# Kernel optimization log

Measured on AMD Instinct MI355X. Metric: run time of the kernel, lower is better.

The kernel has to match this reference:

```python
import jax, jax.numpy as jnp
import numpy as np

B, S, NH, HID, NL = 64, 512, 16, 512, 16
W_WIN, PAD, THR, BW = 5, 2, 5.0, 0.1
D_IN = 1 + 2 * NH


def setup_inputs():
    key = jax.random.key(0)
    ks = jax.random.split(key, 16)
    time = jax.random.uniform(ks[0], (B, S)) * 1000.0
    mag = 15.0 + jax.random.normal(ks[1], (B, S))
    err = 0.01 + 0.1 * jax.random.uniform(ks[2], (B, S))
    sc = 0.05
    p = {}
    p["light_curve"] = jnp.stack([time, mag, err], axis=1)  # (B,3,S)
    p["valid_mask"] = jnp.ones((B, S), dtype=bool)
    p["frequency"] = 0.5 + 4.5 * jax.random.uniform(ks[3], (B,))
    p["W_ih0"] = sc * jax.random.normal(ks[4], (3 * HID, D_IN))
    p["b_ih0"] = jnp.zeros((3 * HID,))
    p["W_hh0"] = sc * jax.random.normal(ks[5], (3 * HID, HID))
    p["b_hh0"] = jnp.zeros((3 * HID,))
    p["W_ih1"] = sc * jax.random.normal(ks[6], (3 * HID, HID))
    p["b_ih1"] = jnp.zeros((3 * HID,))
    p["W_hh1"] = sc * jax.random.normal(ks[7], (3 * HID, HID))
    p["b_hh1"] = jnp.zeros((3 * HID,))
    p["Wl1"] = sc * jax.random.normal(ks[8], (HID, HID))
    p["bl1"] = jnp.zeros((HID,))
    p["Wl2"] = sc * jax.random.normal(ks[9], (NL, HID))
    p["bl2"] = jnp.zeros((NL,))
    return p


def _flag_outliers(phase, mag):
    # Sorted-window weighted (Epanechnikov in circular phase-delta) mean/std outlier test.
    # Caller guarantees all points valid (setup uses an all-True mask), so index_select == identity.
    perm = jnp.argsort(phase)
    ps, ms = phase[perm], mag[perm]

    def windows(x):
        xp = jnp.concatenate([x[-PAD:], x, x[:PAD]])  # circular pad
        return jnp.stack([xp[i:i + S] for i in range(W_WIN)], axis=-1)  # (S, w)

    wp, wm = windows(ps), windows(ms)
    cols = jnp.array([i for i in range(W_WIN) if i != PAD])
    dphi = wp[:, cols] - wp[:, PAD:PAD + 1]
    dphi = jnp.remainder(dphi - 0.5, 1.0) - 0.5
    wgt = 0.75 * (1.0 - dphi ** 2)
    wmm = wm[:, cols]
    wsum = wgt.sum(-1)
    loc = (wmm * wgt).sum(-1) / wsum
    scale = jnp.sqrt((((wmm - loc[:, None]) ** 2) * wgt).sum(-1) / (wsum - 1.0))
    thr = loc + THR * scale
    sigma = jnp.zeros_like(mag).at[perm].set(thr)  # inverse-permute (index_copy_)
    return mag > sigma


def _gru_layer(x, W_ih, b_ih, W_hh, b_hh):
    # torch nn.GRU cell math; x: (B,S,D) -> (B,S,H)
    xW = jnp.einsum('bsd,gd->bsg', x, W_ih) + b_ih  # (B,S,3H)

    def step(h, xt):
        hW = h @ W_hh.T + b_hh
        xr, xz, xn = jnp.split(xt, 3, axis=-1)
        hr, hz, hn = jnp.split(hW, 3, axis=-1)
        r = jax.nn.sigmoid(xr + hr)
        z = jax.nn.sigmoid(xz + hz)
        n = jnp.tanh(xn + r * hn)
        h = (1.0 - z) * n + z * h
        return h, h

    h0 = jnp.zeros((x.shape[0], W_hh.shape[1]), x.dtype)
    _, hs = jax.lax.scan(step, h0, jnp.swapaxes(xW, 0, 1))
    return jnp.swapaxes(hs, 0, 1)


def reference(light_curve, valid_mask, frequency, W_ih0, b_ih0, W_hh0, b_hh0,
              W_ih1, b_ih1, W_hh1, b_hh1, Wl1, bl1, Wl2, bl2):
    time, mag, err = light_curve[:, 0], light_curve[:, 1], light_curve[:, 2]
    period = 2.0 / frequency[:, None]  # fold_with_double_period=True (default)
    phase = jnp.remainder(time, period) / period
    outlier = jax.vmap(_flag_outliers)(phase, mag)
    is_valid = valid_mask & ~outlier

    # periodic-kernel interpolation on 50-point grid; align phase to brightness max
    grid = jnp.linspace(0.0, 1.0, 50)
    delta = grid[None, :, None] - phase[:, None, :]  # (B,50,S)
    K = jnp.exp((jnp.cos(2.0 * jnp.pi * delta) - 1.0) / BW ** 2)
    Wk = is_valid[:, None, :].astype(K.dtype) * K
    Wk = Wk / Wk.sum(-1, keepdims=True)
    smooth = (Wk * mag[:, None, :]).sum(-1)  # (B,50)
    phase = phase - grid[jnp.argmax(smooth, axis=-1)][:, None]

    # sort by phase, invalid points last; scaler=None -> loc 0, scale 1
    big = jnp.finfo(jnp.float32).max
    idx = jnp.argsort(jnp.where(is_valid, phase, big), axis=-1)
    phase = jnp.take_along_axis(phase, idx, -1)
    mag = jnp.take_along_axis(mag, idx, -1)
    is_valid = jnp.take_along_axis(is_valid, idx, -1)

    # Fourier phase embedding [cos_1..cos_H, sin_1..sin_H] + mag -> (B,S,2H+1)
    k = jnp.arange(1, NH + 1, dtype=phase.dtype)
    ang = 2.0 * jnp.pi * phase[:, :, None] * k
    emb = jnp.concatenate([jnp.cos(ang), jnp.sin(ang), mag[:, :, None]], axis=-1)

    ht = _gru_layer(emb, W_ih0, b_ih0, W_hh0, b_hh0)
    ht = _gru_layer(ht, W_ih1, b_ih1, W_hh1, b_hh1)

    m = is_valid[:, :, None].astype(ht.dtype)  # context='average'
    ctx = (ht * m).sum(1) / m.sum(1)
    h1 = jax.nn.gelu(ctx @ Wl1.T + bl1, approximate=False)
    z = h1 @ Wl2.T + bl2
    return z
```

## Files before the change

### kernel.cpp

```cpp
#include <hip/hip_runtime.h>


typedef unsigned short u16;
typedef unsigned int u32;
typedef unsigned long long u64;

__device__ __forceinline__ float b2f(u16 u) { return __uint_as_float(((u32)u) << 16); }
__device__ __forceinline__ float blo(u32 u) { return __uint_as_float(u << 16); }
__device__ __forceinline__ float bhi(u32 u) { return __uint_as_float(u & 0xffff0000u); }
__device__ __forceinline__ u16 f2b(float f) {
    u32 x = __float_as_uint(f);
    u32 r = x + 0x7fffu + ((x >> 16) & 1u);
    return (u16)(r >> 16);
}

#define SS 512
#define TWO_PI 6.28318530717958647692f
#define BIGF 3.402823466e+38f
#define PANEL_ELEMS (1536 * 512)
#define FLAGS_BYTES 32768
#define FL(g, f) (((g) * 16 + (f)) * 16)
#define F_A 0
#define F_B 2
#define F_C 4
#define G_A 6
#define G_B 8
#define G_C 10
#define F_PRE 12
#define F_CTX 14

struct P {
    const void* lc;
    const void* freq;
    const void* W[12];
    void* out;
    void* ws;
    unsigned long long ws_size;
};

__device__ __forceinline__ bool inputs_are_bf16(const void* freq) {
    const u16* q = (const u16*)freq;
    bool ok = true;
    for (int i = 0; i < 64; ++i) {
        float v = b2f(q[i]);
        ok = ok && (v >= 0.4f) && (v <= 5.5f);
    }
    return ok;
}

template<bool BF>
__device__ __forceinline__ float ldw(const void* p, size_t i) {
    if constexpr (BF) return b2f(((const u16*)p)[i]);
    else              return ((const float*)p)[i];
}
template<bool BF>
__device__ __forceinline__ const void* rowp(const void* base, int row) {
    if constexpr (BF) return (const void*)((const u16*)base + (size_t)row * 512);
    else              return (const void*)((const float*)base + (size_t)row * 512);
}

__device__ __forceinline__ void sc_store_f(float* ptr, float v) {
    __hip_atomic_store(ptr, v, __ATOMIC_RELAXED, __HIP_MEMORY_SCOPE_AGENT);
}
__device__ __forceinline__ float sc_load_f(const float* ptr) {
    return __hip_atomic_load(ptr, __ATOMIC_RELAXED, __HIP_MEMORY_SCOPE_AGENT);
}
__device__ __forceinline__ void sc_store_i(int* ptr, int v) {
    __hip_atomic_store(ptr, v, __ATOMIC_RELAXED, __HIP_MEMORY_SCOPE_AGENT);
}
__device__ __forceinline__ int sc_load_i(const int* ptr) {
    return __hip_atomic_load(ptr, __ATOMIC_RELAXED, __HIP_MEMORY_SCOPE_AGENT);
}
__device__ __forceinline__ void waitge(const int* f, int v, int* dead) {
    if (*dead) return;
    int it = 0;
    while (sc_load_i(f) < v) {
        __builtin_amdgcn_s_sleep(1);
        if (++it > 2000000) { *dead = 1; break; }
    }
}

template<bool BF>
__device__ void build_panel_one(const void* W, int tid, char* panbase) {
    if constexpr (BF) {
        const uint4* Ws = (const uint4*)W;
        uint4* panel = (uint4*)panbase;
        for (int i = tid; i < 1536 * 64; i += 512) {
            int r = i >> 6, k8 = i & 63;
            panel[(size_t)k8 * 1536 + r] = Ws[i];
        }
    } else {
        const float4* Ws = (const float4*)W;
        float4* panel = (float4*)panbase;
        for (int i = tid; i < 1536 * 128; i += 512) {
            int r = i >> 7, k4 = i & 127;
            panel[(size_t)k4 * 1536 + r] = Ws[i];
        }
    }
}
template<bool BF>
__device__ void build_piece(const void* W, int half, int tid, char* panbase) {
    if constexpr (BF) {
        const uint4* Ws = (const uint4*)W;
        uint4* panel = (uint4*)panbase;
        for (int i = tid; i < 768 * 64; i += 512) {
            int r768 = i >> 6, k8 = i & 63;
            int g3 = r768 >> 8, r = r768 & 255;
            int srcrow = g3 * 512 + half * 256 + r;
            panel[(size_t)k8 * 768 + r768] = Ws[(size_t)srcrow * 64 + k8];
        }
    } else {
        const float4* Ws = (const float4*)W;
        float4* panel = (float4*)panbase;
        for (int i = tid; i < 768 * 128; i += 512) {
            int r768 = i >> 7, k4 = i & 127;
            int g3 = r768 >> 8, r = r768 & 255;
            int srcrow = g3 * 512 + half * 256 + r;
            panel[(size_t)k4 * 768 + r768] = Ws[(size_t)srcrow * 128 + k4];
        }
    }
}

template<bool BF>
__device__ __forceinline__ void tridot_panel(const void* panel, int j,
                                             const float* __restrict__ sh,
                                             float& ar, float& az, float& an) {
    if constexpr (BF) {
        const uint4* pr = (const uint4*)panel + j;
        const uint4* pz = pr + 512;
        const uint4* pn = pr + 1024;
        for (int k0 = 0; k0 < 512; k0 += 8) {
            size_t o = (size_t)(k0 >> 3) * 1536;
            float4 h0 = *(const float4*)&sh[k0];
            float4 h1 = *(const float4*)&sh[k0 + 4];
            uint4 a = pr[o], c = pz[o], d = pn[o];
            ar += blo(a.x) * h0.x + bhi(a.x) * h0.y + blo(a.y) * h0.z + bhi(a.y) * h0.w
                + blo(a.z) * h1.x + bhi(a.z) * h1.y + blo(a.w) * h1.z + bhi(a.w) * h1.w;
            az += blo(c.x) * h0.x + bhi(c.x) * h0.y + blo(c.y) * h0.z + bhi(c.y) * h0.w
                + blo(c.z) * h1.x + bhi(c.z) * h1.y + blo(c.w) * h1.z + bhi(c.w) * h1.w;
            an += blo(d.x) * h0.x + bhi(d.x) * h0.y + blo(d.y) * h0.z + bhi(d.y) * h0.w
                + blo(d.z) * h1.x + bhi(d.z) * h1.y + blo(d.w) * h1.z + bhi(d.w) * h1.w;
        }
    } else {
        const float4* pr = (const float4*)panel + j;
        const float4* pz = pr + 512;
        const float4* pn = pr + 1024;
        for (int k0 = 0; k0 < 512; k0 += 8) {
            size_t o = (size_t)(k0 >> 2) * 1536;
            float4 h0 = *(const float4*)&sh[k0];
            float4 h1 = *(const float4*)&sh[k0 + 4];
            float4 a0 = pr[o], a1 = pr[o + 1536];
            float4 c0 = pz[o], c1 = pz[o + 1536];
            float4 d0 = pn[o], d1 = pn[o + 1536];
            ar += a0.x * h0.x + a0.y * h0.y + a0.z * h0.z + a0.w * h0.w
                + a1.x * h1.x + a1.y * h1.y + a1.z * h1.z + a1.w * h1.w;
            az += c0.x * h0.x + c0.y * h0.y + c0.z * h0.z + c0.w * h0.w
                + c1.x * h1.x + c1.y * h1.y + c1.z * h1.z + c1.w * h1.w;
            an += d0.x * h0.x + d0.y * h0.y + d0.z * h0.z + d0.w * h0.w
                + d1.x * h1.x + d1.y * h1.y + d1.z * h1.z + d1.w * h1.w;
        }
    }
}

template<bool BF>
__device__ __forceinline__ void tridot_piece(const void* panel, int r,
                                             const float* __restrict__ sh,
                                             float& ar, float& az, float& an) {
    if constexpr (BF) {
        const uint4* pr = (const uint4*)panel + r;
        const uint4* pz = pr + 256;
        const uint4* pn = pr + 512;
        for (int k0 = 0; k0 < 512; k0 += 8) {
            size_t o = (size_t)(k0 >> 3) * 768;
            float4 h0 = *(const float4*)&sh[k0];
            float4 h1 = *(const float4*)&sh[k0 + 4];
            uint4 a = pr[o], c = pz[o], d = pn[o];
            ar += blo(a.x) * h0.x + bhi(a.x) * h0.y + blo(a.y) * h0.z + bhi(a.y) * h0.w
                + blo(a.z) * h1.x + bhi(a.z) * h1.y + blo(a.w) * h1.z + bhi(a.w) * h1.w;
            az += blo(c.x) * h0.x + bhi(c.x) * h0.y + blo(c.y) * h0.z + bhi(c.y) * h0.w
                + blo(c.z) * h1.x + bhi(c.z) * h1.y + blo(c.w) * h1.z + bhi(c.w) * h1.w;
            an += blo(d.x) * h0.x + bhi(d.x) * h0.y + blo(d.y) * h0.z + bhi(d.y) * h0.w
                + blo(d.z) * h1.x + bhi(d.z) * h1.y + blo(d.w) * h1.z + bhi(d.w) * h1.w;
        }
    } else {
        const float4* pr = (const float4*)panel + r;
        const float4* pz = pr + 256;
        const float4* pn = pr + 512;
        for (int k0 = 0; k0 < 512; k0 += 8) {
            size_t o = (size_t)(k0 >> 2) * 768;
            float4 h0 = *(const float4*)&sh[k0];
            float4 h1 = *(const float4*)&sh[k0 + 4];
            float4 a0 = pr[o], a1 = pr[o + 768];
            float4 c0 = pz[o], c1 = pz[o + 768];
            float4 d0 = pn[o], d1 = pn[o + 768];
            ar += a0.x * h0.x + a0.y * h0.y + a0.z * h0.z + a0.w * h0.w
                + a1.x * h1.x + a1.y * h1.y + a1.z * h1.z + a1.w * h1.w;
            az += c0.x * h0.x + c0.y * h0.y + c0.z * h0.z + c0.w * h0.w
                + c1.x * h1.x + c1.y * h1.y + c1.z * h1.z + c1.w * h1.w;
            an += d0.x * h0.x + d0.y * h0.y + d0.z * h0.z + d0.w * h0.w
                + d1.x * h1.x + d1.y * h1.y + d1.z * h1.z + d1.w * h1.w;
        }
    }
}

template<bool BF>
__device__ __forceinline__ float dot512(const void* vr, const float* __restrict__ sh) {
    float acc = 0.f;
    if constexpr (BF) {
        const u32* pr = (const u32*)vr;
        for (int k0 = 0; k0 < 512; k0 += 8) {
            float4 h0 = *(const float4*)&sh[k0];
            float4 h1 = *(const float4*)&sh[k0 + 4];
            uint4 a = *(const uint4*)(pr + (k0 >> 1));
            acc += blo(a.x) * h0.x + bhi(a.x) * h0.y + blo(a.y) * h0.z + bhi(a.y) * h0.w
                 + blo(a.z) * h1.x + bhi(a.z) * h1.y + blo(a.w) * h1.z + bhi(a.w) * h1.w;
        }
    } else {
        const float* pr = (const float*)vr;
        for (int k0 = 0; k0 < 512; k0 += 8) {
            float4 h0 = *(const float4*)&sh[k0];
            float4 h1 = *(const float4*)&sh[k0 + 4];
            float4 a0 = *(const float4*)(pr + k0), a1 = *(const float4*)(pr + k0 + 4);
            acc += a0.x * h0.x + a0.y * h0.y + a0.z * h0.z + a0.w * h0.w
                 + a1.x * h1.x + a1.y * h1.y + a1.z * h1.z + a1.w * h1.w;
        }
    }
    return acc;
}

struct PreShm {
    float ph[512], mg[512], skey[512], sig[512], vld[512];
    int   sidx[512];
    float ps2[512], ms2[512], vs2[512];
    float pn[50][8], pd[50][8], smoothv[50];
    float gshift, nv;
};

__device__ void bitonic512(float* skey, int* sidx, int tid) {
    for (int k = 2; k <= 512; k <<= 1) {
        for (int j = k >> 1; j > 0; j >>= 1) {
            int ixj = tid ^ j;
            if (ixj > tid) {
                float ka = skey[tid], kb = skey[ixj];
                int ia = sidx[tid], ib = sidx[ixj];
                bool up = ((tid & k) == 0);
                bool agtb = (ka > kb) || (ka == kb && ia > ib);
                if (agtb == up) {
                    skey[tid] = kb; skey[ixj] = ka;
                    sidx[tid] = ib; sidx[ixj] = ia;
                }
            }
            __syncthreads();
        }
    }
}

template<bool BF>
__device__ void preproc_core(const P& p, PreShm& s, int b, int tid) {
    float period = 2.0f / ldw<BF>(p.freq, b);
    float t = ldw<BF>(p.lc, (size_t)b * 3 * SS + tid);
    float m = ldw<BF>(p.lc, (size_t)b * 3 * SS + SS + tid);
    float ph0 = fmodf(t, period) / period;
    s.ph[tid] = ph0; s.mg[tid] = m;
    s.skey[tid] = ph0; s.sidx[tid] = tid;
    __syncthreads();
    bitonic512(s.skey, s.sidx, tid);
    {
        float pc = s.skey[tid];
        float wv[4], mv[4];
        float wsum = 0.f, wm = 0.f;
        const int offs[4] = {-2, -1, 1, 2};
#pragma unroll
        for (int c = 0; c < 4; ++c) {
            int jj = (tid + offs[c]) & 511;
            float d = s.skey[jj] - pc;
            float u = d - 0.5f; u = u - floorf(u);
            float dphi = u - 0.5f;
            float w = 0.75f * (1.0f - dphi * dphi);
            float mm = s.mg[s.sidx[jj]];
            wv[c] = w; mv[c] = mm;
            wsum += w; wm += w * mm;
        }
        float loc = wm / wsum;
        float s2 = 0.f;
#pragma unroll
        for (int c = 0; c < 4; ++c) { float dm = mv[c] - loc; s2 += dm * dm * wv[c]; }
        float scale = sqrtf(s2 / (wsum - 1.0f));
        s.sig[s.sidx[tid]] = loc + 5.0f * scale;
    }
    __syncthreads();
    s.vld[tid] = (s.mg[tid] > s.sig[tid]) ? 0.0f : 1.0f;
    __syncthreads();
    if (tid == 0) {
        float acc = 0.f;
        for (int i = 0; i < 512; ++i) acc += s.vld[i];
        s.nv = acc;
    }
    {
        int g = tid >> 3, pq = tid & 7;
        if (g < 50) {
            float gv = (float)g * (1.0f / 49.0f);
            float num = 0.f, den = 0.f;
            int s0 = pq * 64;
            for (int ss = s0; ss < s0 + 64; ++ss) {
                float d = gv - s.ph[ss];
                float c = cosf(TWO_PI * d);
                float K = expf((c - 1.0f) * 100.0f);
                float w = s.vld[ss] * K;
                den += w; num += w * s.mg[ss];
            }
            s.pn[g][pq] = num; s.pd[g][pq] = den;
        }
    }
    __syncthreads();
    if (tid < 50) {
        float num = 0.f, den = 0.f;
#pragma unroll
        for (int c = 0; c < 8; ++c) { num += s.pn[tid][c]; den += s.pd[tid][c]; }
        s.smoothv[tid] = num / den;
    }
    __syncthreads();
    if (tid == 0) {
        float best = s.smoothv[0]; int bi = 0;
        for (int g = 1; g < 50; ++g) if (s.smoothv[g] > best) { best = s.smoothv[g]; bi = g; }
        s.gshift = (float)bi * (1.0f / 49.0f);
    }
    __syncthreads();
    float p2 = s.ph[tid] - s.gshift;
    s.ph[tid] = p2;
    s.skey[tid] = (s.vld[tid] > 0.f) ? p2 : BIGF;
    s.sidx[tid] = tid;
    __syncthreads();
    bitonic512(s.skey, s.sidx, tid);
    {
        int o = s.sidx[tid];
        s.ps2[tid] = s.ph[o]; s.ms2[tid] = s.mg[o]; s.vs2[tid] = s.vld[o];
    }
    __syncthreads();
}

struct ShmA { PreShm pre; float psb[2][512], msb[2][512]; float h0L[1024]; float eL[2][34]; };
struct ShmB { float h0loc[1024]; };
struct ShmC { float h1L[1024]; float vs2L[2][512]; float nvL[2]; float ctxL[512], gL[512]; };
struct ShmOldA { PreShm pre; float h0[512], h1[512], eL[34]; };
struct ShmU {
    union { ShmA a; ShmB b; ShmC c; ShmOldA o; } u;
    int dead;
};

template<bool BF, bool PAN>
__device__ void run_all(const P& p, ShmU& S) {
    PreShm& pre = S.u.o.pre;
    float* h0 = S.u.o.h0;
    float* h1 = S.u.o.h1;
    float* eL = S.u.o.eL;
    int b = blockIdx.x, tid = threadIdx.x;
    char* panbase = (char*)p.ws + FLAGS_BYTES;
    const size_t PMAT = (size_t)PANEL_ELEMS * (BF ? 2 : 4);

    if constexpr (PAN) {
        build_panel_one<BF>(p.W[2], tid, panbase);
        build_panel_one<BF>(p.W[4], tid, panbase + PMAT);
        build_panel_one<BF>(p.W[6], tid, panbase + 2 * PMAT);
        __threadfence();
    }
    preproc_core<BF>(p, pre, b, tid);

    int j = tid;
    float wr0[33], wz0[33], wn0[33];
#pragma unroll
    for (int d = 0; d < 33; ++d) {
        wr0[d] = ldw<BF>(p.W[0], (size_t)j * 33 + d);
        wz0[d] = ldw<BF>(p.W[0], ((size_t)j + 512) * 33 + d);
        wn0[d] = ldw<BF>(p.W[0], ((size_t)j + 1024) * 33 + d);
    }
    float bi0r = ldw<BF>(p.W[1], j), bi0z = ldw<BF>(p.W[1], j + 512), bi0n = ldw<BF>(p.W[1], j + 1024);
    float bh0r = ldw<BF>(p.W[3], j), bh0z = ldw<BF>(p.W[3], j + 512), bh0n = ldw<BF>(p.W[3], j + 1024);
    float bi1r = ldw<BF>(p.W[5], j), bi1z = ldw<BF>(p.W[5], j + 512), bi1n = ldw<BF>(p.W[5], j + 1024);
    float bh1r = ldw<BF>(p.W[7], j), bh1z = ldw<BF>(p.W[7], j + 512), bh1n = ldw<BF>(p.W[7], j + 1024);

    const void* pan0  = (const void*)panbase;
    const void* pan1x = (const void*)(panbase + PMAT);
    const void* pan1h = (const void*)(panbase + 2 * PMAT);
    const void *w0r = rowp<BF>(p.W[2], j), *w0z = rowp<BF>(p.W[2], j + 512), *w0n = rowp<BF>(p.W[2], j + 1024);
    const void *x1r = rowp<BF>(p.W[4], j), *x1z = rowp<BF>(p.W[4], j + 512), *x1n = rowp<BF>(p.W[4], j + 1024);
    const void *w1r = rowp<BF>(p.W[6], j), *w1z = rowp<BF>(p.W[6], j + 512), *w1n = rowp<BF>(p.W[6], j + 1024);

    h0[j] = 0.f; h1[j] = 0.f;
    float cacc = 0.f;
    __syncthreads();

    for (int tt = 0; tt < 512; ++tt) {
        if (j < 16) {
            float ang = TWO_PI * pre.ps2[tt] * (float)(j + 1);
            float sv, cv; sincosf(ang, &sv, &cv);
            eL[j] = cv; eL[16 + j] = sv;
        }
        if (j == 32) eL[32] = pre.ms2[tt];
        __syncthreads();
        float xr = bi0r, xz = bi0z, xn = bi0n;
#pragma unroll
        for (int d = 0; d < 33; ++d) {
            float e = eL[d];
            xr += wr0[d] * e; xz += wz0[d] * e; xn += wn0[d] * e;
        }
        float ar = bh0r, az = bh0z, an = bh0n;
        if constexpr (PAN) tridot_panel<BF>(pan0, j, h0, ar, az, an);
        else {
            for (int k = 0; k < 512; ++k) {
                float h = h0[k];
                ar += ldw<BF>(w0r, k) * h; az += ldw<BF>(w0z, k) * h; an += ldw<BF>(w0n, k) * h;
            }
        }
        float h0prev = h0[j];
        float r0 = 1.0f / (1.0f + expf(-(xr + ar)));
        float z0 = 1.0f / (1.0f + expf(-(xz + az)));
        float n0 = tanhf(xn + r0 * an);
        float nh0 = (1.0f - z0) * n0 + z0 * h0prev;
        __syncthreads();
        h0[j] = nh0;
        __syncthreads();
        float yr = bi1r, yz = bi1z, yn = bi1n;
        float cr = bh1r, cz = bh1z, cn = bh1n;
        if constexpr (PAN) {
            tridot_panel<BF>(pan1x, j, h0, yr, yz, yn);
            tridot_panel<BF>(pan1h, j, h1, cr, cz, cn);
        } else {
            for (int k = 0; k < 512; ++k) {
                float h = h0[k], g = h1[k];
                yr += ldw<BF>(x1r, k) * h; yz += ldw<BF>(x1z, k) * h; yn += ldw<BF>(x1n, k) * h;
                cr += ldw<BF>(w1r, k) * g; cz += ldw<BF>(w1z, k) * g; cn += ldw<BF>(w1n, k) * g;
            }
        }
        float h1prev = h1[j];
        float r1 = 1.0f / (1.0f + expf(-(yr + cr)));
        float z1 = 1.0f / (1.0f + expf(-(yz + cz)));
        float n1 = tanhf(yn + r1 * cn);
        float nh1 = (1.0f - z1) * n1 + z1 * h1prev;
        cacc += pre.vs2[tt] * nh1;
        __syncthreads();
        h1[j] = nh1;
    }
    __syncthreads();

    h0[j] = cacc / pre.nv;
    __syncthreads();
    float a1 = ldw<BF>(p.W[9], j) + dot512<BF>(rowp<BF>(p.W[8], j), h0);
    float g = 0.5f * a1 * (1.0f + erff(a1 * 0.70710678118654752440f));
    __syncthreads();
    h1[j] = g;
    __syncthreads();
    if (j < 16) {
        float a2 = ldw<BF>(p.W[11], j) + dot512<BF>(rowp<BF>(p.W[10], j), h1);
        if constexpr (BF) ((u16*)p.out)[(size_t)b * 16 + j] = f2b(a2);
        else              ((float*)p.out)[(size_t)b * 16 + j] = a2;
    }
}

__global__ __launch_bounds__(512) void fused_kernel_old(P p) {
    __shared__ ShmU S;
    bool bf = inputs_are_bf16(p.freq);
    u64 PMAT = bf ? 1572864ull : 3145728ull;
    bool pan = (p.ws && p.ws_size >= (u64)FLAGS_BYTES + 3 * PMAT);
    if (bf) { if (pan) run_all<true, true>(p, S);  else run_all<true, false>(p, S); }
    else    { if (pan) run_all<false, true>(p, S); else run_all<false, false>(p, S); }
}


template<bool BF>
__device__ void runA(const P& p, ShmU& S, int g, int hf, int tid, char* pan,
                     float* h0r, float* pp, int* flags) {
    build_piece<BF>(p.W[2], hf, tid, pan);
    __threadfence();
    int myb = 2 * g + hf, ob = 2 * g + (1 - hf);
    preproc_core<BF>(p, S.u.a.pre, myb, tid);
    sc_store_f(&pp[(size_t)myb * 2048 + tid], S.u.a.pre.ps2[tid]);
    sc_store_f(&pp[(size_t)myb * 2048 + 512 + tid], S.u.a.pre.ms2[tid]);
    sc_store_f(&pp[(size_t)myb * 2048 + 1024 + tid], S.u.a.pre.vs2[tid]);
    if (tid == 0) sc_store_f(&pp[(size_t)myb * 2048 + 1536], S.u.a.pre.nv);
    asm volatile("s_waitcnt vmcnt(0)" ::: "memory");
    __syncthreads();
    if (tid == 0) sc_store_i(&flags[FL(g, F_PRE + hf)], 1);
    S.u.a.psb[hf][tid] = S.u.a.pre.ps2[tid];
    S.u.a.msb[hf][tid] = S.u.a.pre.ms2[tid];
    if (tid == 0) waitge(&flags[FL(g, F_PRE + (1 - hf))], 1, &S.dead);
    __syncthreads();
    S.u.a.psb[1 - hf][tid] = sc_load_f(&pp[(size_t)ob * 2048 + tid]);
    S.u.a.msb[1 - hf][tid] = sc_load_f(&pp[(size_t)ob * 2048 + 512 + tid]);

    const int r = tid & 255, bb = tid >> 8;
    const int j = hf * 256 + r;
    float wr0[33], wz0[33], wn0[33];
#pragma unroll
    for (int d = 0; d < 33; ++d) {
        wr0[d] = ldw<BF>(p.W[0], (size_t)j * 33 + d);
        wz0[d] = ldw<BF>(p.W[0], ((size_t)j + 512) * 33 + d);
        wn0[d] = ldw<BF>(p.W[0], ((size_t)j + 1024) * 33 + d);
    }
    float bi0r = ldw<BF>(p.W[1], j), bi0z = ldw<BF>(p.W[1], j + 512), bi0n = ldw<BF>(p.W[1], j + 1024);
    float bh0r = ldw<BF>(p.W[3], j), bh0z = ldw<BF>(p.W[3], j + 512), bh0n = ldw<BF>(p.W[3], j + 1024);

    S.u.a.h0L[tid] = 0.f; S.u.a.h0L[tid + 512] = 0.f;
    __syncthreads();

    for (int t = 0; t < 512; ++t) {
        if (t > 0) {
            if (tid == 0) waitge(&flags[FL(g, F_A + (1 - hf))], t, &S.dead);
            __syncthreads();
            S.u.a.h0L[bb * 512 + (1 - hf) * 256 + r] =
                sc_load_f(&h0r[(size_t)g * 2048 + ((t - 1) & 1) * 1024 + (1 - hf) * 512 + bb * 256 + r]);
            __syncthreads();
            if (tid == 0) sc_store_i(&flags[FL(g, G_A + hf)], t);
        }
        if (tid < 16) {
            float ang = TWO_PI * S.u.a.psb[0][t] * (float)(tid + 1);
            float sv, cv; sincosf(ang, &sv, &cv);
            S.u.a.eL[0][tid] = cv; S.u.a.eL[0][16 + tid] = sv;
        } else if (tid < 32) {
            int k = tid - 16;
            float ang = TWO_PI * S.u.a.psb[1][t] * (float)(k + 1);
            float sv, cv; sincosf(ang, &sv, &cv);
            S.u.a.eL[1][k] = cv; S.u.a.eL[1][16 + k] = sv;
        }
        if (tid == 32) S.u.a.eL[0][32] = S.u.a.msb[0][t];
        if (tid == 33) S.u.a.eL[1][32] = S.u.a.msb[1][t];
        __syncthreads();
        float xr = bi0r, xz = bi0z, xn = bi0n;
#pragma unroll
        for (int d = 0; d < 33; ++d) {
            float e = S.u.a.eL[bb][d];
            xr += wr0[d] * e; xz += wz0[d] * e; xn += wn0[d] * e;
        }
        float ar = bh0r, az = bh0z, an = bh0n;
        tridot_piece<BF>(pan, r, &S.u.a.h0L[bb * 512], ar, az, an);
        float h0prev = S.u.a.h0L[bb * 512 + j];
        float r0 = 1.0f / (1.0f + expf(-(xr + ar)));
        float z0 = 1.0f / (1.0f + expf(-(xz + az)));
        float n0 = tanhf(xn + r0 * an);
        float nh0 = (1.0f - z0) * n0 + z0 * h0prev;
        __syncthreads();
        S.u.a.h0L[bb * 512 + j] = nh0;
        if (tid == 0 && t >= 2) {
            waitge(&flags[FL(g, G_A + (1 - hf))], t - 1, &S.dead);
            waitge(&flags[FL(g, G_B + 0)], t - 1, &S.dead);
            waitge(&flags[FL(g, G_B + 1)], t - 1, &S.dead);
        }
        __syncthreads();
        sc_store_f(&h0r[(size_t)g * 2048 + (t & 1) * 1024 + hf * 512 + bb * 256 + r], nh0);
        asm volatile("s_waitcnt vmcnt(0)" ::: "memory");
        __syncthreads();
        if (tid == 0) sc_store_i(&flags[FL(g, F_A + hf)], t + 1);
    }
}

template<bool BF>
__device__ void runB(const P& p, ShmU& S, int g, int hf, int tid, char* pan,
                     float* h0r, float* yrng, int* flags) {
    build_piece<BF>(p.W[4], hf, tid, pan);
    __threadfence();
    __syncthreads();
    const int r = tid & 255, bb = tid >> 8;
    const int j = hf * 256 + r;
    float bi1r = ldw<BF>(p.W[5], j), bi1z = ldw<BF>(p.W[5], j + 512), bi1n = ldw<BF>(p.W[5], j + 1024);

    for (int t = 0; t < 512; ++t) {
        if (tid == 0) {
            waitge(&flags[FL(g, F_A + 0)], t + 1, &S.dead);
            waitge(&flags[FL(g, F_A + 1)], t + 1, &S.dead);
        }
        __syncthreads();
        S.u.b.h0loc[bb * 512 + r] =
            sc_load_f(&h0r[(size_t)g * 2048 + (t & 1) * 1024 + 0 * 512 + bb * 256 + r]);
        S.u.b.h0loc[bb * 512 + 256 + r] =
            sc_load_f(&h0r[(size_t)g * 2048 + (t & 1) * 1024 + 1 * 512 + bb * 256 + r]);
        __syncthreads();
        if (tid == 0) sc_store_i(&flags[FL(g, G_B + hf)], t + 1);
        float yr = bi1r, yz = bi1z, yn = bi1n;
        tridot_piece<BF>(pan, r, &S.u.b.h0loc[bb * 512], yr, yz, yn);
        if (tid == 0 && t >= 2) waitge(&flags[FL(g, G_C + hf)], t - 1, &S.dead);
        __syncthreads();
        float* slot = &yrng[(size_t)g * 6144 + (t & 1) * 3072 + hf * 1536];
        sc_store_f(&slot[bb * 256 + r], yr);
        sc_store_f(&slot[512 + bb * 256 + r], yz);
        sc_store_f(&slot[1024 + bb * 256 + r], yn);
        asm volatile("s_waitcnt vmcnt(0)" ::: "memory");
        __syncthreads();
        if (tid == 0) sc_store_i(&flags[FL(g, F_B + hf)], t + 1);
    }
}

template<bool BF>
__device__ void runC(const P& p, ShmU& S, int g, int hf, int tid, char* pan,
                     float* yrng, float* h1r, float* pp, float* ctxb, int* flags) {
    build_piece<BF>(p.W[6], hf, tid, pan);
    __threadfence();
    if (tid == 0) {
        waitge(&flags[FL(g, F_PRE + 0)], 1, &S.dead);
        waitge(&flags[FL(g, F_PRE + 1)], 1, &S.dead);
    }
    __syncthreads();
    S.u.c.vs2L[0][tid] = sc_load_f(&pp[(size_t)(2 * g) * 2048 + 1024 + tid]);
    S.u.c.vs2L[1][tid] = sc_load_f(&pp[(size_t)(2 * g + 1) * 2048 + 1024 + tid]);
    if (tid == 0) {
        S.u.c.nvL[0] = sc_load_f(&pp[(size_t)(2 * g) * 2048 + 1536]);
        S.u.c.nvL[1] = sc_load_f(&pp[(size_t)(2 * g + 1) * 2048 + 1536]);
    }
    S.u.c.h1L[tid] = 0.f; S.u.c.h1L[tid + 512] = 0.f;
    __syncthreads();

    const int r = tid & 255, bb = tid >> 8;
    const int j = hf * 256 + r;
    float bh1r = ldw<BF>(p.W[7], j), bh1z = ldw<BF>(p.W[7], j + 512), bh1n = ldw<BF>(p.W[7], j + 1024);
    float cacc = 0.f;

    for (int t = 0; t < 512; ++t) {
        if (tid == 0) {
            waitge(&flags[FL(g, F_B + hf)], t + 1, &S.dead);
            if (t > 0) waitge(&flags[FL(g, F_C + (1 - hf))], t, &S.dead);
        }
        __syncthreads();
        if (t > 0) {
            S.u.c.h1L[bb * 512 + (1 - hf) * 256 + r] =
                sc_load_f(&h1r[(size_t)g * 2048 + ((t - 1) & 1) * 1024 + (1 - hf) * 512 + bb * 256 + r]);
        }
        const float* slot = &yrng[(size_t)g * 6144 + (t & 1) * 3072 + hf * 1536];
        float yr = sc_load_f(&slot[bb * 256 + r]);
        float yz = sc_load_f(&slot[512 + bb * 256 + r]);
        float yn = sc_load_f(&slot[1024 + bb * 256 + r]);
        __syncthreads();
        if (tid == 0) sc_store_i(&flags[FL(g, G_C + hf)], t + 1);
        float cr = bh1r, cz = bh1z, cn = bh1n;
        tridot_piece<BF>(pan, r, &S.u.c.h1L[bb * 512], cr, cz, cn);
        float h1prev = S.u.c.h1L[bb * 512 + j];
        float r1 = 1.0f / (1.0f + expf(-(yr + cr)));
        float z1 = 1.0f / (1.0f + expf(-(yz + cz)));
        float n1 = tanhf(yn + r1 * cn);
        float nh1 = (1.0f - z1) * n1 + z1 * h1prev;
        cacc += S.u.c.vs2L[bb][t] * nh1;
        __syncthreads();
        S.u.c.h1L[bb * 512 + j] = nh1;
        if (tid == 0 && t >= 2) waitge(&flags[FL(g, G_C + (1 - hf))], t - 1, &S.dead);
        __syncthreads();
        sc_store_f(&h1r[(size_t)g * 2048 + (t & 1) * 1024 + hf * 512 + bb * 256 + r], nh1);
        asm volatile("s_waitcnt vmcnt(0)" ::: "memory");
        __syncthreads();
        if (tid == 0) sc_store_i(&flags[FL(g, F_C + hf)], t + 1);
    }

    sc_store_f(&ctxb[(size_t)g * 1024 + hf * 512 + bb * 256 + r], cacc);
    asm volatile("s_waitcnt vmcnt(0)" ::: "memory");
    __syncthreads();
    if (tid == 0) {
        sc_store_i(&flags[FL(g, F_CTX + hf)], 1);
        waitge(&flags[FL(g, F_CTX + (1 - hf))], 1, &S.dead);
    }
    __syncthreads();
    float nv = S.u.c.nvL[hf];
    S.u.c.ctxL[tid] = sc_load_f(&ctxb[(size_t)g * 1024 + (tid >> 8) * 512 + hf * 256 + (tid & 255)]) / nv;
    __syncthreads();
    float a1 = ldw<BF>(p.W[9], tid) + dot512<BF>(rowp<BF>(p.W[8], tid), S.u.c.ctxL);
    float gg = 0.5f * a1 * (1.0f + erff(a1 * 0.70710678118654752440f));
    __syncthreads();
    S.u.c.gL[tid] = gg;
    __syncthreads();
    if (tid < 16) {
        float a2 = ldw<BF>(p.W[11], tid) + dot512<BF>(rowp<BF>(p.W[10], tid), S.u.c.gL);
        int hb = 2 * g + hf;
        if constexpr (BF) ((u16*)p.out)[(size_t)hb * 16 + tid] = f2b(a2);
        else              ((float*)p.out)[(size_t)hb * 16 + tid] = a2;
    }
}

template<bool BF>
__device__ void run_pipe(const P& p, ShmU& S) {
    const int bid = blockIdx.x;
    const int piece = bid & 7;
    if (piece >= 6) return;
    const int g = bid >> 3;
    const int role = piece >> 1, hf = piece & 1;
    const int tid = threadIdx.x;
    if (tid == 0) S.dead = 0;
    __syncthreads();

    char* wsb = (char*)p.ws;
    int* flags = (int*)wsb;
    const size_t PIECE = BF ? 786432 : 1572864;
    char* pans = wsb + FLAGS_BYTES;
    char* mypan = pans + (size_t)piece * PIECE;
    float* h0r  = (float*)(pans + 6 * PIECE);
    float* yrng = h0r + (size_t)32 * 2048;
    float* h1r  = yrng + (size_t)32 * 6144;
    float* pp   = h1r + (size_t)32 * 2048;
    float* ctxb = pp + (size_t)64 * 2048;

    if (role == 0)      runA<BF>(p, S, g, hf, tid, mypan, h0r, pp, flags);
    else if (role == 1) runB<BF>(p, S, g, hf, tid, mypan, h0r, yrng, flags);
    else                runC<BF>(p, S, g, hf, tid, mypan, yrng, h1r, pp, ctxb, flags);
}

__global__ __launch_bounds__(512) void fused_kernel_pipe(P p) {
    __shared__ ShmU S;
    if (inputs_are_bf16(p.freq)) run_pipe<true>(p, S);
    else                         run_pipe<false>(p, S);
}

extern "C" void kernel_launch(void* const* d_in, const int* in_sizes, int n_in,
                              void* d_out, int out_size, void* d_ws, size_t ws_size,
                              hipStream_t stream) {
    P p;
    p.lc = d_in[0];
    p.freq = d_in[2];
    for (int i = 0; i < 12; ++i) p.W[i] = d_in[3 + i];
    p.out = d_out;
    p.ws = d_ws;
    p.ws_size = (unsigned long long)ws_size;

    const size_t need_pipe = 11436032ull;
    if (d_ws && ws_size >= need_pipe) {
        hipMemsetAsync(d_ws, 0, FLAGS_BYTES, stream);
        fused_kernel_pipe<<<256, 512, 0, stream>>>(p);
    } else {
        fused_kernel_old<<<64, 512, 0, stream>>>(p);
    }
    (void)in_sizes; (void)n_in; (void)out_size;
}
```

Before: 14.31 ms.

## Split recurrent dot over K halves so each panel load serves both batch rows

In the three GRU stages, threads used to each own one batch row and stream the full 512-long weight column from the panel. Now the two thread halves split the K dimension, and each computes partial dots for both batch rows from the same panel load. The partial sums are combined through shared memory, and one half then runs the gate math for both rows. This halves redundant weight-panel traffic per step at the cost of an extra shared-memory reduction and a barrier. It also moves the layer-0 input weights from register arrays to per-step loads, spreads the flag waits across several threads, and shortens the deadlock timeout.

```diff
diff --git a/kernel.cpp b/kernel.cpp
--- a/kernel.cpp
+++ b/kernel.cpp
@@ -76,7 +76,7 @@
     int it = 0;
     while (sc_load_i(f) < v) {
         __builtin_amdgcn_s_sleep(1);
-        if (++it > 2000000) { *dead = 1; break; }
+        if (++it > 400000) { *dead = 1; break; }
     }
 }
 
@@ -163,42 +163,61 @@
 }
 
 template<bool BF>
-__device__ __forceinline__ void tridot_piece(const void* panel, int r,
-                                             const float* __restrict__ sh,
-                                             float& ar, float& az, float& an) {
+__device__ __forceinline__ void tridot2(const void* panel, int r, int kh,
+                                        const float* __restrict__ ha,
+                                        const float* __restrict__ hb,
+                                        float& a0r, float& a0z, float& a0n,
+                                        float& a1r, float& a1z, float& a1n) {
+    const int kbeg = kh * 256;
     if constexpr (BF) {
         const uint4* pr = (const uint4*)panel + r;
         const uint4* pz = pr + 256;
         const uint4* pn = pr + 512;
-        for (int k0 = 0; k0 < 512; k0 += 8) {
+        for (int k0 = kbeg; k0 < kbeg + 256; k0 += 8) {
             size_t o = (size_t)(k0 >> 3) * 768;
-            float4 h0 = *(const float4*)&sh[k0];
-            float4 h1 = *(const float4*)&sh[k0 + 4];
+            float4 ha0 = *(const float4*)&ha[k0];
+            float4 ha1 = *(const float4*)&ha[k0 + 4];
+            float4 hb0 = *(const float4*)&hb[k0];
+            float4 hb1 = *(const float4*)&hb[k0 + 4];
             uint4 a = pr[o], c = pz[o], d = pn[o];
-            ar += blo(a.x) * h0.x + bhi(a.x) * h0.y + blo(a.y) * h0.z + bhi(a.y) * h0.w
-                + blo(a.z) * h1.x + bhi(a.z) * h1.y + blo(a.w) * h1.z + bhi(a.w) * h1.w;
-            az += blo(c.x) * h0.x + bhi(c.x) * h0.y + blo(c.y) * h0.z + bhi(c.y) * h0.w
-                + blo(c.z) * h1.x + bhi(c.z) * h1.y + blo(c.w) * h1.z + bhi(c.w) * h1.w;
-            an += blo(d.x) * h0.x + bhi(d.x) * h0.y + blo(d.y) * h0.z + bhi(d.y) * h0.w
-                + blo(d.z) * h1.x + bhi(d.z) * h1.y + blo(d.w) * h1.z + bhi(d.w) * h1.w;
+            a0r += blo(a.x)*ha0.x + bhi(a.x)*ha0.y + blo(a.y)*ha0.z + bhi(a.y)*ha0.w
+                 + blo(a.z)*ha1.x + bhi(a.z)*ha1.y + blo(a.w)*ha1.z + bhi(a.w)*ha1.w;
+            a1r += blo(a.x)*hb0.x + bhi(a.x)*hb0.y + blo(a.y)*hb0.z + bhi(a.y)*hb0.w
+                 + blo(a.z)*hb1.x + bhi(a.z)*hb1.y + blo(a.w)*hb1.z + bhi(a.w)*hb1.w;
+            a0z += blo(c.x)*ha0.x + bhi(c.x)*ha0.y + blo(c.y)*ha0.z + bhi(c.y)*ha0.w
+                 + blo(c.z)*ha1.x + bhi(c.z)*ha1.y + blo(c.w)*ha1.z + bhi(c.w)*ha1.w;
+            a1z += blo(c.x)*hb0.x + bhi(c.x)*hb0.y + blo(c.y)*hb0.z + bhi(c.y)*hb0.w
+                 + blo(c.z)*hb1.x + bhi(c.z)*hb1.y + blo(c.w)*hb1.z + bhi(c.w)*hb1.w;
+            a0n += blo(d.x)*ha0.x + bhi(d.x)*ha0.y + blo(d.y)*ha0.z + bhi(d.y)*ha0.w
+                 + blo(d.z)*ha1.x + bhi(d.z)*ha1.y + blo(d.w)*ha1.z + bhi(d.w)*ha1.w;
+            a1n += blo(d.x)*hb0.x + bhi(d.x)*hb0.y + blo(d.y)*hb0.z + bhi(d.y)*hb0.w
+                 + blo(d.z)*hb1.x + bhi(d.z)*hb1.y + blo(d.w)*hb1.z + bhi(d.w)*hb1.w;
         }
     } else {
         const float4* pr = (const float4*)panel + r;
         const float4* pz = pr + 256;
         const float4* pn = pr + 512;
-        for (int k0 = 0; k0 < 512; k0 += 8) {
+        for (int k0 = kbeg; k0 < kbeg + 256; k0 += 8) {
             size_t o = (size_t)(k0 >> 2) * 768;
-            float4 h0 = *(const float4*)&sh[k0];
-            float4 h1 = *(const float4*)&sh[k0 + 4];
+            float4 ha0 = *(const float4*)&ha[k0];
+            float4 ha1 = *(const float4*)&ha[k0 + 4];
+            float4 hb0 = *(const float4*)&hb[k0];
+            float4 hb1 = *(const float4*)&hb[k0 + 4];
             float4 a0 = pr[o], a1 = pr[o + 768];
             float4 c0 = pz[o], c1 = pz[o + 768];
             float4 d0 = pn[o], d1 = pn[o + 768];
-            ar += a0.x * h0.x + a0.y * h0.y + a0.z * h0.z + a0.w * h0.w
-                + a1.x * h1.x + a1.y * h1.y + a1.z * h1.z + a1.w * h1.w;
-            az += c0.x * h0.x + c0.y * h0.y + c0.z * h0.z + c0.w * h0.w
-                + c1.x * h1.x + c1.y * h1.y + c1.z * h1.z + c1.w * h1.w;
-            an += d0.x * h0.x + d0.y * h0.y + d0.z * h0.z + d0.w * h0.w
-                + d1.x * h1.x + d1.y * h1.y + d1.z * h1.z + d1.w * h1.w;
+            a0r += a0.x*ha0.x + a0.y*ha0.y + a0.z*ha0.z + a0.w*ha0.w
+                 + a1.x*ha1.x + a1.y*ha1.y + a1.z*ha1.z + a1.w*ha1.w;
+            a1r += a0.x*hb0.x + a0.y*hb0.y + a0.z*hb0.z + a0.w*hb0.w
+                 + a1.x*hb1.x + a1.y*hb1.y + a1.z*hb1.z + a1.w*hb1.w;
+            a0z += c0.x*ha0.x + c0.y*ha0.y + c0.z*ha0.z + c0.w*ha0.w
+                 + c1.x*ha1.x + c1.y*ha1.y + c1.z*ha1.z + c1.w*ha1.w;
+            a1z += c0.x*hb0.x + c0.y*hb0.y + c0.z*hb0.z + c0.w*hb0.w
+                 + c1.x*hb1.x + c1.y*hb1.y + c1.z*hb1.z + c1.w*hb1.w;
+            a0n += d0.x*ha0.x + d0.y*ha0.y + d0.z*ha0.z + d0.w*ha0.w
+                 + d1.x*ha1.x + d1.y*ha1.y + d1.z*ha1.z + d1.w*ha1.w;
+            a1n += d0.x*hb0.x + d0.y*hb0.y + d0.z*hb0.z + d0.w*hb0.w
+                 + d1.x*hb1.x + d1.y*hb1.y + d1.z*hb1.z + d1.w*hb1.w;
         }
     }
 }
@@ -339,9 +358,19 @@
     __syncthreads();
 }
 
-struct ShmA { PreShm pre; float psb[2][512], msb[2][512]; float h0L[1024]; float eL[2][34]; };
-struct ShmB { float h0loc[1024]; };
-struct ShmC { float h1L[1024]; float vs2L[2][512]; float nvL[2]; float ctxL[512], gL[512]; };
+struct ShmA {
+    PreShm pre;
+    float psb[2][512], msb[2][512];
+    float h0L[1024];
+    float eL[2][34];
+    float part[6][256];
+    float xp[3][256];
+};
+struct ShmB { float h0loc[1024]; float part[6][256]; };
+struct ShmC {
+    float h1L[1024]; float vs2L[2][512]; float nvL[2];
+    float ctxL[512], gL[512]; float part[6][256];
+};
 struct ShmOldA { PreShm pre; float h0[512], h1[512], eL[34]; };
 struct ShmU {
     union { ShmA a; ShmB b; ShmC c; ShmOldA o; } u;
@@ -470,6 +499,7 @@
 template<bool BF>
 __device__ void runA(const P& p, ShmU& S, int g, int hf, int tid, char* pan,
                      float* h0r, float* pp, int* flags) {
+    int* dead = &S.dead;
     build_piece<BF>(p.W[2], hf, tid, pan);
     __threadfence();
     int myb = 2 * g + hf, ob = 2 * g + (1 - hf);
@@ -483,32 +513,26 @@
     if (tid == 0) sc_store_i(&flags[FL(g, F_PRE + hf)], 1);
     S.u.a.psb[hf][tid] = S.u.a.pre.ps2[tid];
     S.u.a.msb[hf][tid] = S.u.a.pre.ms2[tid];
-    if (tid == 0) waitge(&flags[FL(g, F_PRE + (1 - hf))], 1, &S.dead);
+    if (tid == 0) waitge(&flags[FL(g, F_PRE + (1 - hf))], 1, dead);
     __syncthreads();
     S.u.a.psb[1 - hf][tid] = sc_load_f(&pp[(size_t)ob * 2048 + tid]);
     S.u.a.msb[1 - hf][tid] = sc_load_f(&pp[(size_t)ob * 2048 + 512 + tid]);
 
-    const int r = tid & 255, bb = tid >> 8;
+    const int r = tid & 255, kh = tid >> 8;
     const int j = hf * 256 + r;
-    float wr0[33], wz0[33], wn0[33];
-#pragma unroll
-    for (int d = 0; d < 33; ++d) {
-        wr0[d] = ldw<BF>(p.W[0], (size_t)j * 33 + d);
-        wz0[d] = ldw<BF>(p.W[0], ((size_t)j + 512) * 33 + d);
-        wn0[d] = ldw<BF>(p.W[0], ((size_t)j + 1024) * 33 + d);
-    }
-    float bi0r = ldw<BF>(p.W[1], j), bi0z = ldw<BF>(p.W[1], j + 512), bi0n = ldw<BF>(p.W[1], j + 1024);
-    float bh0r = ldw<BF>(p.W[3], j), bh0z = ldw<BF>(p.W[3], j + 512), bh0n = ldw<BF>(p.W[3], j + 1024);
-
-    S.u.a.h0L[tid] = 0.f; S.u.a.h0L[tid + 512] = 0.f;
+    const float bi0r = ldw<BF>(p.W[1], j), bi0z = ldw<BF>(p.W[1], j + 512), bi0n = ldw<BF>(p.W[1], j + 1024);
+    const float bh0r = ldw<BF>(p.W[3], j), bh0z = ldw<BF>(p.W[3], j + 512), bh0n = ldw<BF>(p.W[3], j + 1024);
+
+    float* h0L = S.u.a.h0L;
+    h0L[tid] = 0.f; h0L[tid + 512] = 0.f;
     __syncthreads();
 
     for (int t = 0; t < 512; ++t) {
         if (t > 0) {
-            if (tid == 0) waitge(&flags[FL(g, F_A + (1 - hf))], t, &S.dead);
+            if (tid == 0) waitge(&flags[FL(g, F_A + (1 - hf))], t, dead);
             __syncthreads();
-            S.u.a.h0L[bb * 512 + (1 - hf) * 256 + r] =
-                sc_load_f(&h0r[(size_t)g * 2048 + ((t - 1) & 1) * 1024 + (1 - hf) * 512 + bb * 256 + r]);
+            h0L[kh * 512 + (1 - hf) * 256 + r] =
+                sc_load_f(&h0r[(size_t)g * 2048 + ((t - 1) & 1) * 1024 + (1 - hf) * 512 + kh * 256 + r]);
             __syncthreads();
             if (tid == 0) sc_store_i(&flags[FL(g, G_A + hf)], t);
         }
@@ -525,28 +549,54 @@
         if (tid == 32) S.u.a.eL[0][32] = S.u.a.msb[0][t];
         if (tid == 33) S.u.a.eL[1][32] = S.u.a.msb[1][t];
         __syncthreads();
+
         float xr = bi0r, xz = bi0z, xn = bi0n;
 #pragma unroll
         for (int d = 0; d < 33; ++d) {
-            float e = S.u.a.eL[bb][d];
-            xr += wr0[d] * e; xz += wz0[d] * e; xn += wn0[d] * e;
-        }
-        float ar = bh0r, az = bh0z, an = bh0n;
-        tridot_piece<BF>(pan, r, &S.u.a.h0L[bb * 512], ar, az, an);
-        float h0prev = S.u.a.h0L[bb * 512 + j];
-        float r0 = 1.0f / (1.0f + expf(-(xr + ar)));
-        float z0 = 1.0f / (1.0f + expf(-(xz + az)));
-        float n0 = tanhf(xn + r0 * an);
-        float nh0 = (1.0f - z0) * n0 + z0 * h0prev;
-        __syncthreads();
-        S.u.a.h0L[bb * 512 + j] = nh0;
-        if (tid == 0 && t >= 2) {
-            waitge(&flags[FL(g, G_A + (1 - hf))], t - 1, &S.dead);
-            waitge(&flags[FL(g, G_B + 0)], t - 1, &S.dead);
-            waitge(&flags[FL(g, G_B + 1)], t - 1, &S.dead);
-        }
-        __syncthreads();
-        sc_store_f(&h0r[(size_t)g * 2048 + (t & 1) * 1024 + hf * 512 + bb * 256 + r], nh0);
+            float e = S.u.a.eL[kh][d];
+            xr += ldw<BF>(p.W[0], (size_t)j * 33 + d) * e;
+            xz += ldw<BF>(p.W[0], ((size_t)j + 512) * 33 + d) * e;
+            xn += ldw<BF>(p.W[0], ((size_t)j + 1024) * 33 + d) * e;
+        }
+        float p0r = 0.f, p0z = 0.f, p0n = 0.f, p1r = 0.f, p1z = 0.f, p1n = 0.f;
+        tridot2<BF>(pan, r, kh, &h0L[0], &h0L[512], p0r, p0z, p0n, p1r, p1z, p1n);
+        if (kh == 1) {
+            S.u.a.part[0][r] = p0r; S.u.a.part[1][r] = p0z; S.u.a.part[2][r] = p0n;
+            S.u.a.part[3][r] = p1r; S.u.a.part[4][r] = p1z; S.u.a.part[5][r] = p1n;
+            S.u.a.xp[0][r] = xr; S.u.a.xp[1][r] = xz; S.u.a.xp[2][r] = xn;
+        }
+        __syncthreads();
+        float nh00 = 0.f, nh01 = 0.f;
+        if (kh == 0) {
+            float ar0 = bh0r + p0r + S.u.a.part[0][r];
+            float az0 = bh0z + p0z + S.u.a.part[1][r];
+            float an0 = bh0n + p0n + S.u.a.part[2][r];
+            float ar1 = bh0r + p1r + S.u.a.part[3][r];
+            float az1 = bh0z + p1z + S.u.a.part[4][r];
+            float an1 = bh0n + p1n + S.u.a.part[5][r];
+            float x1r = S.u.a.xp[0][r], x1z = S.u.a.xp[1][r], x1n = S.u.a.xp[2][r];
+            float h0p0 = h0L[j], h0p1 = h0L[512 + j];
+            float r0 = 1.f / (1.f + expf(-(xr + ar0)));
+            float z0 = 1.f / (1.f + expf(-(xz + az0)));
+            float n0 = tanhf(xn + r0 * an0);
+            nh00 = (1.f - z0) * n0 + z0 * h0p0;
+            float r1 = 1.f / (1.f + expf(-(x1r + ar1)));
+            float z1 = 1.f / (1.f + expf(-(x1z + az1)));
+            float n1 = tanhf(x1n + r1 * an1);
+            nh01 = (1.f - z1) * n1 + z1 * h0p1;
+            h0L[j] = nh00; h0L[512 + j] = nh01;
+        }
+        if (t >= 2) {
+            if (tid == 0) waitge(&flags[FL(g, G_A + (1 - hf))], t - 1, dead);
+            if (tid == 1) waitge(&flags[FL(g, G_B + 0)], t - 1, dead);
+            if (tid == 2) waitge(&flags[FL(g, G_B + 1)], t - 1, dead);
+        }
+        __syncthreads();
+        if (kh == 0) {
+            float* dst = &h0r[(size_t)g * 2048 + (t & 1) * 1024 + hf * 512];
+            sc_store_f(&dst[r], nh00);
+            sc_store_f(&dst[256 + r], nh01);
+        }
         asm volatile("s_waitcnt vmcnt(0)" ::: "memory");
         __syncthreads();
         if (tid == 0) sc_store_i(&flags[FL(g, F_A + hf)], t + 1);
@@ -556,33 +606,44 @@
 template<bool BF>
 __device__ void runB(const P& p, ShmU& S, int g, int hf, int tid, char* pan,
                      float* h0r, float* yrng, int* flags) {
+    int* dead = &S.dead;
     build_piece<BF>(p.W[4], hf, tid, pan);
     __threadfence();
     __syncthreads();
-    const int r = tid & 255, bb = tid >> 8;
+    const int r = tid & 255, kh = tid >> 8;
     const int j = hf * 256 + r;
-    float bi1r = ldw<BF>(p.W[5], j), bi1z = ldw<BF>(p.W[5], j + 512), bi1n = ldw<BF>(p.W[5], j + 1024);
+    const float bi1r = ldw<BF>(p.W[5], j), bi1z = ldw<BF>(p.W[5], j + 512), bi1n = ldw<BF>(p.W[5], j + 1024);
+    float* h0loc = S.u.b.h0loc;
 
     for (int t = 0; t < 512; ++t) {
-        if (tid == 0) {
-            waitge(&flags[FL(g, F_A + 0)], t + 1, &S.dead);
-            waitge(&flags[FL(g, F_A + 1)], t + 1, &S.dead);
-        }
-        __syncthreads();
-        S.u.b.h0loc[bb * 512 + r] =
-            sc_load_f(&h0r[(size_t)g * 2048 + (t & 1) * 1024 + 0 * 512 + bb * 256 + r]);
-        S.u.b.h0loc[bb * 512 + 256 + r] =
-            sc_load_f(&h0r[(size_t)g * 2048 + (t & 1) * 1024 + 1 * 512 + bb * 256 + r]);
+        if (tid == 0) waitge(&flags[FL(g, F_A + 0)], t + 1, dead);
+        if (tid == 1) waitge(&flags[FL(g, F_A + 1)], t + 1, dead);
+        __syncthreads();
+        const float* src = &h0r[(size_t)g * 2048 + (t & 1) * 1024];
+        h0loc[kh * 512 + r]       = sc_load_f(&src[0 * 512 + kh * 256 + r]);
+        h0loc[kh * 512 + 256 + r] = sc_load_f(&src[1 * 512 + kh * 256 + r]);
         __syncthreads();
         if (tid == 0) sc_store_i(&flags[FL(g, G_B + hf)], t + 1);
-        float yr = bi1r, yz = bi1z, yn = bi1n;
-        tridot_piece<BF>(pan, r, &S.u.b.h0loc[bb * 512], yr, yz, yn);
-        if (tid == 0 && t >= 2) waitge(&flags[FL(g, G_C + hf)], t - 1, &S.dead);
-        __syncthreads();
-        float* slot = &yrng[(size_t)g * 6144 + (t & 1) * 3072 + hf * 1536];
-        sc_store_f(&slot[bb * 256 + r], yr);
-        sc_store_f(&slot[512 + bb * 256 + r], yz);
-        sc_store_f(&slot[1024 + bb * 256 + r], yn);
+        float p0r = 0.f, p0z = 0.f, p0n = 0.f, p1r = 0.f, p1z = 0.f, p1n = 0.f;
+        tridot2<BF>(pan, r, kh, &h0loc[0], &h0loc[512], p0r, p0z, p0n, p1r, p1z, p1n);
+        if (kh == 1) {
+            S.u.b.part[0][r] = p0r; S.u.b.part[1][r] = p0z; S.u.b.part[2][r] = p0n;
+            S.u.b.part[3][r] = p1r; S.u.b.part[4][r] = p1z; S.u.b.part[5][r] = p1n;
+        }
+        if (tid == 0 && t >= 2) waitge(&flags[FL(g, G_C + hf)], t - 1, dead);
+        __syncthreads();
+        if (kh == 0) {
+            float y0r = bi1r + p0r + S.u.b.part[0][r];
+            float y0z = bi1z + p0z + S.u.b.part[1][r];
+            float y0n = bi1n + p0n + S.u.b.part[2][r];
+            float y1r = bi1r + p1r + S.u.b.part[3][r];
+            float y1z = bi1z + p1z + S.u.b.part[4][r];
+            float y1n = bi1n + p1n + S.u.b.part[5][r];
+            float* slot = &yrng[(size_t)g * 6144 + (t & 1) * 3072 + hf * 1536];
+            sc_store_f(&slot[r], y0r);         sc_store_f(&slot[256 + r], y1r);
+            sc_store_f(&slot[512 + r], y0z);   sc_store_f(&slot[768 + r], y1z);
+            sc_store_f(&slot[1024 + r], y0n);  sc_store_f(&slot[1280 + r], y1n);
+        }
         asm volatile("s_waitcnt vmcnt(0)" ::: "memory");
         __syncthreads();
         if (tid == 0) sc_store_i(&flags[FL(g, F_B + hf)], t + 1);
@@ -592,12 +653,11 @@
 template<bool BF>
 __device__ void runC(const P& p, ShmU& S, int g, int hf, int tid, char* pan,
                      float* yrng, float* h1r, float* pp, float* ctxb, int* flags) {
+    int* dead = &S.dead;
     build_piece<BF>(p.W[6], hf, tid, pan);
     __threadfence();
-    if (tid == 0) {
-        waitge(&flags[FL(g, F_PRE + 0)], 1, &S.dead);
-        waitge(&flags[FL(g, F_PRE + 1)], 1, &S.dead);
-    }
+    if (tid == 0) waitge(&flags[FL(g, F_PRE + 0)], 1, dead);
+    if (tid == 1) waitge(&flags[FL(g, F_PRE + 1)], 1, dead);
     __syncthreads();
     S.u.c.vs2L[0][tid] = sc_load_f(&pp[(size_t)(2 * g) * 2048 + 1024 + tid]);
     S.u.c.vs2L[1][tid] = sc_load_f(&pp[(size_t)(2 * g + 1) * 2048 + 1024 + tid]);
@@ -605,54 +665,81 @@
         S.u.c.nvL[0] = sc_load_f(&pp[(size_t)(2 * g) * 2048 + 1536]);
         S.u.c.nvL[1] = sc_load_f(&pp[(size_t)(2 * g + 1) * 2048 + 1536]);
     }
-    S.u.c.h1L[tid] = 0.f; S.u.c.h1L[tid + 512] = 0.f;
-    __syncthreads();
-
-    const int r = tid & 255, bb = tid >> 8;
+    float* h1L = S.u.c.h1L;
+    h1L[tid] = 0.f; h1L[tid + 512] = 0.f;
+    __syncthreads();
+
+    const int r = tid & 255, kh = tid >> 8;
     const int j = hf * 256 + r;
-    float bh1r = ldw<BF>(p.W[7], j), bh1z = ldw<BF>(p.W[7], j + 512), bh1n = ldw<BF>(p.W[7], j + 1024);
-    float cacc = 0.f;
+    const float bh1r = ldw<BF>(p.W[7], j), bh1z = ldw<BF>(p.W[7], j + 512), bh1n = ldw<BF>(p.W[7], j + 1024);
+    float cacc0 = 0.f, cacc1 = 0.f;
 
     for (int t = 0; t < 512; ++t) {
-        if (tid == 0) {
-            waitge(&flags[FL(g, F_B + hf)], t + 1, &S.dead);
-            if (t > 0) waitge(&flags[FL(g, F_C + (1 - hf))], t, &S.dead);
-        }
+        if (tid == 0) waitge(&flags[FL(g, F_B + hf)], t + 1, dead);
+        if (t > 0 && tid == 1) waitge(&flags[FL(g, F_C + (1 - hf))], t, dead);
         __syncthreads();
         if (t > 0) {
-            S.u.c.h1L[bb * 512 + (1 - hf) * 256 + r] =
-                sc_load_f(&h1r[(size_t)g * 2048 + ((t - 1) & 1) * 1024 + (1 - hf) * 512 + bb * 256 + r]);
-        }
-        const float* slot = &yrng[(size_t)g * 6144 + (t & 1) * 3072 + hf * 1536];
-        float yr = sc_load_f(&slot[bb * 256 + r]);
-        float yz = sc_load_f(&slot[512 + bb * 256 + r]);
-        float yn = sc_load_f(&slot[1024 + bb * 256 + r]);
+            h1L[kh * 512 + (1 - hf) * 256 + r] =
+                sc_load_f(&h1r[(size_t)g * 2048 + ((t - 1) & 1) * 1024 + (1 - hf) * 512 + kh * 256 + r]);
+        }
+        float y0r = 0.f, y0z = 0.f, y0n = 0.f, y1r = 0.f, y1z = 0.f, y1n = 0.f;
+        if (kh == 0) {
+            const float* slot = &yrng[(size_t)g * 6144 + (t & 1) * 3072 + hf * 1536];
+            y0r = sc_load_f(&slot[r]);         y1r = sc_load_f(&slot[256 + r]);
+            y0z = sc_load_f(&slot[512 + r]);   y1z = sc_load_f(&slot[768 + r]);
+            y0n = sc_load_f(&slot[1024 + r]);  y1n = sc_load_f(&slot[1280 + r]);
+        }
         __syncthreads();
         if (tid == 0) sc_store_i(&flags[FL(g, G_C + hf)], t + 1);
-        float cr = bh1r, cz = bh1z, cn = bh1n;
-        tridot_piece<BF>(pan, r, &S.u.c.h1L[bb * 512], cr, cz, cn);
-        float h1prev = S.u.c.h1L[bb * 512 + j];
-        float r1 = 1.0f / (1.0f + expf(-(yr + cr)));
-        float z1 = 1.0f / (1.0f + expf(-(yz + cz)));
-        float n1 = tanhf(yn + r1 * cn);
-        float nh1 = (1.0f - z1) * n1 + z1 * h1prev;
-        cacc += S.u.c.vs2L[bb][t] * nh1;
-        __syncthreads();
-        S.u.c.h1L[bb * 512 + j] = nh1;
-        if (tid == 0 && t >= 2) waitge(&flags[FL(g, G_C + (1 - hf))], t - 1, &S.dead);
-        __syncthreads();
-        sc_store_f(&h1r[(size_t)g * 2048 + (t & 1) * 1024 + hf * 512 + bb * 256 + r], nh1);
+        float p0r = 0.f, p0z = 0.f, p0n = 0.f, p1r = 0.f, p1z = 0.f, p1n = 0.f;
+        tridot2<BF>(pan, r, kh, &h1L[0], &h1L[512], p0r, p0z, p0n, p1r, p1z, p1n);
+        if (kh == 1) {
+            S.u.c.part[0][r] = p0r; S.u.c.part[1][r] = p0z; S.u.c.part[2][r] = p0n;
+            S.u.c.part[3][r] = p1r; S.u.c.part[4][r] = p1z; S.u.c.part[5][r] = p1n;
+        }
+        __syncthreads();
+        float nh10 = 0.f, nh11 = 0.f;
+        if (kh == 0) {
+            float cr0 = bh1r + p0r + S.u.c.part[0][r];
+            float cz0 = bh1z + p0z + S.u.c.part[1][r];
+            float cn0 = bh1n + p0n + S.u.c.part[2][r];
+            float cr1 = bh1r + p1r + S.u.c.part[3][r];
+            float cz1 = bh1z + p1z + S.u.c.part[4][r];
+            float cn1 = bh1n + p1n + S.u.c.part[5][r];
+            float h1p0 = h1L[j], h1p1 = h1L[512 + j];
+            float r0 = 1.f / (1.f + expf(-(y0r + cr0)));
+            float z0 = 1.f / (1.f + expf(-(y0z + cz0)));
+            float n0 = tanhf(y0n + r0 * cn0);
+            nh10 = (1.f - z0) * n0 + z0 * h1p0;
+            float r1 = 1.f / (1.f + expf(-(y1r + cr1)));
+            float z1 = 1.f / (1.f + expf(-(y1z + cz1)));
+            float n1 = tanhf(y1n + r1 * cn1);
+            nh11 = (1.f - z1) * n1 + z1 * h1p1;
+            cacc0 += S.u.c.vs2L[0][t] * nh10;
+            cacc1 += S.u.c.vs2L[1][t] * nh11;
+            h1L[j] = nh10; h1L[512 + j] = nh11;
+        }
+        if (t >= 2 && tid == 2) waitge(&flags[FL(g, G_C + (1 - hf))], t, dead);
+        __syncthreads();
+        if (kh == 0) {
+            float* dst = &h1r[(size_t)g * 2048 + (t & 1) * 1024 + hf * 512];
+            sc_store_f(&dst[r], nh10);
+            sc_store_f(&dst[256 + r], nh11);
+        }
         asm volatile("s_waitcnt vmcnt(0)" ::: "memory");
         __syncthreads();
         if (tid == 0) sc_store_i(&flags[FL(g, F_C + hf)], t + 1);
     }
 
-    sc_store_f(&ctxb[(size_t)g * 1024 + hf * 512 + bb * 256 + r], cacc);
+    if (kh == 0) {
+        sc_store_f(&ctxb[(size_t)g * 1024 + hf * 512 + r], cacc0);
+        sc_store_f(&ctxb[(size_t)g * 1024 + hf * 512 + 256 + r], cacc1);
+    }
     asm volatile("s_waitcnt vmcnt(0)" ::: "memory");
     __syncthreads();
     if (tid == 0) {
         sc_store_i(&flags[FL(g, F_CTX + hf)], 1);
-        waitge(&flags[FL(g, F_CTX + (1 - hf))], 1, &S.dead);
+        waitge(&flags[FL(g, F_CTX + (1 - hf))], 1, dead);
     }
     __syncthreads();
     float nv = S.u.c.nvL[hf];
```

After: 12.44 ms. -13.1%, faster.
